# Performance work log

Hardware: AMD Instinct MI355X
Metric: run time of the kernel (lower is better)

Reference implementation:

```python
import jax, jax.numpy as jnp
import numpy as np

B, D, H = 262144, 8, 64  # batch, in_out_dim, hidden_dim


def _lin_init(k, fan_in, fan_out):
    k1, k2 = jax.random.split(k)
    s = 1.0 / np.sqrt(fan_in)
    W = jax.random.uniform(k1, (fan_in, fan_out), minval=-s, maxval=s, dtype=jnp.float32)
    b = jax.random.uniform(k2, (fan_out,), minval=-s, maxval=s, dtype=jnp.float32)
    return W, b


def setup_inputs():
    key = jax.random.key(0)
    ks = jax.random.split(key, 12)
    w1_0, b1_0 = _lin_init(ks[0], D + 1, H)
    w1_1, b1_1 = _lin_init(ks[1], H, H)
    w1_2, b1_2 = _lin_init(ks[2], H, H)
    w1_o, b1_o = _lin_init(ks[3], H, D)
    w2_0, b2_0 = _lin_init(ks[4], D + 1, H)
    w2_1, b2_1 = _lin_init(ks[5], H, H)
    w2_2, b2_2 = _lin_init(ks[6], H, H)
    w2_o, b2_o = _lin_init(ks[7], H, 1)
    t = jax.random.uniform(ks[8], (), dtype=jnp.float32)
    z = jax.random.normal(ks[9], (B, D), dtype=jnp.float32)
    logp_z = jnp.zeros((B, 1), dtype=jnp.float32)
    return dict(t=t, z=z, logp_z=logp_z,
                w1_0=w1_0, b1_0=b1_0, w1_1=w1_1, b1_1=b1_1, w1_2=w1_2, b1_2=b1_2,
                w1_o=w1_o, b1_o=b1_o,
                w2_0=w2_0, b2_0=b2_0, w2_1=w2_1, b2_1=b2_1, w2_2=w2_2, b2_2=b2_2,
                w2_o=w2_o, b2_o=b2_o)


def reference(t, z, logp_z,
              w1_0, b1_0, w1_1, b1_1, w1_2, b1_2, w1_o, b1_o,
              w2_0, b2_0, w2_1, b2_1, w2_2, b2_2, w2_o, b2_o):
    Bz, Dz = z.shape
    tcol = jnp.full((Bz, 1), t, dtype=z.dtype)  # t repeated per-sample, detached constant

    def net1(zz):  # HyperNetwork1: dz/dt field, Tanh MLP, (B,D+1)->(B,D)
        s = jnp.concatenate([tcol, zz], axis=1)
        x = jnp.tanh(s @ w1_0 + b1_0)
        x = jnp.tanh(x @ w1_1 + b1_1)
        x = jnp.tanh(x @ w1_2 + b1_2)
        return x @ w1_o + b1_o

    dz_dt = net1(z)

    # HyperNetwork2: growth term g, (B,D+1)->(B,1)
    s = jnp.concatenate([tcol, z], axis=1)
    x = jnp.tanh(s @ w2_0 + b2_0)
    x = jnp.tanh(x @ w2_1 + b2_1)
    x = jnp.tanh(x @ w2_2 + b2_2)
    g = x @ w2_o + b2_o

    # Exact trace of d(dz_dt)/dz via D forward-mode JVPs (vectorized, replaces
    # the per-dim autograd.grad loop in trace_df_dz).
    eye = jnp.eye(Dz, dtype=z.dtype)
    jv = jax.vmap(lambda e: jax.jvp(net1, (z,), (jnp.broadcast_to(e, z.shape),))[1])(eye)  # (D,B,D)
    trace = jnp.diagonal(jv, axis1=0, axis2=2).sum(-1)  # (B,)

    dlogp_z_dt = g - trace[:, None]
    return (dz_dt, dlogp_z_dt, g)
```

## Files before the change

kernel.cpp:

```cpp
#include <hip/hip_runtime.h>


#define BATCH 262144

typedef _Float16 h16;
typedef __attribute__((ext_vector_type(2))) __fp16 f16x2;
typedef __attribute__((ext_vector_type(8))) _Float16 half8;
typedef __attribute__((ext_vector_type(4))) float f32x4;

#define MFMA16(a, b, c) __builtin_amdgcn_mfma_f32_16x16x32_f16((a), (b), (c), 0, 0, 0)

#define WS_A   0
#define WS_WO  61440
#define WS_E   62464
#define WS_B   64512
#define WS_BO  66048

__device__ __forceinline__ float tanh_fast(float x) {
    float e = __builtin_amdgcn_exp2f(x * 2.8853900817779268f);
    return 1.0f - 2.0f * __builtin_amdgcn_rcpf(e + 1.0f);
}

__global__ void __launch_bounds__(256) prep(
    const float* __restrict__ w1_0, const float* __restrict__ w1_1,
    const float* __restrict__ w1_2, const float* __restrict__ w1_o,
    const float* __restrict__ w2_0, const float* __restrict__ w2_1,
    const float* __restrict__ w2_2, const float* __restrict__ w2_o,
    const float* __restrict__ b1_0, const float* __restrict__ b1_1,
    const float* __restrict__ b1_2, const float* __restrict__ b1_o,
    const float* __restrict__ b2_0, const float* __restrict__ b2_1,
    const float* __restrict__ b2_2, char* __restrict__ ws)
{
    int t = blockIdx.x * 256 + threadIdx.x;
    if (t < 3840) {
        int slot = t >> 6, lane = t & 63;
        int mrow = lane & 15, kg = lane >> 4;
        half8 v;
        #pragma unroll
        for (int kk = 0; kk < 8; ++kk) {
            int mt = 0, ks = 0;
            float val = 0.0f;
            if (slot < 4) {
                mt = slot; int k = kg * 8 + kk; int m = mt * 16 + mrow;
                val = (k < 9) ? w1_0[k * 64 + m] : 0.0f;
            } else if (slot < 12) {
                int s = slot - 4; mt = s >> 1; ks = s & 1;
                int k = ks * 32 + kg * 8 + kk; int m = mt * 16 + mrow;
                val = w1_1[k * 64 + m];
            } else if (slot < 20) {
                int s = slot - 12; mt = s >> 1; ks = s & 1;
                int k = ks * 32 + kg * 8 + kk; int m = mt * 16 + mrow;
                val = w1_2[k * 64 + m];
            } else if (slot < 22) {
                ks = slot - 20; int k = ks * 32 + kg * 8 + kk;
                val = (mrow < 8) ? w1_o[k * 8 + mrow] : 0.0f;
            } else if (slot < 26) {
                mt = slot - 22; int k = kg * 8 + kk; int m = mt * 16 + mrow;
                val = (k < 9) ? w2_0[k * 64 + m] : 0.0f;
            } else if (slot < 34) {
                int s = slot - 26; mt = s >> 1; ks = s & 1;
                int k = ks * 32 + kg * 8 + kk; int m = mt * 16 + mrow;
                val = w2_1[k * 64 + m];
            } else if (slot < 42) {
                int s = slot - 34; mt = s >> 1; ks = s & 1;
                int k = ks * 32 + kg * 8 + kk; int m = mt * 16 + mrow;
                val = w2_2[k * 64 + m];
            } else if (slot < 44) {
                ks = slot - 42; int k = ks * 32 + kg * 8 + kk;
                val = (mrow == 0) ? w2_o[k] : 0.0f;
            } else if (slot < 52) {
                int s = slot - 44; mt = s >> 1; ks = s & 1;
                int k = ks * 32 + kg * 8 + kk; int m = mt * 16 + mrow;
                val = w1_2[m * 64 + k];
            } else {
                int s = slot - 52; mt = s >> 1; ks = s & 1;
                int k = ks * 32 + kg * 8 + kk; int m = mt * 16 + mrow;
                val = w1_1[m * 64 + k];
            }
            v[kk] = (h16)val;
        }
        *(half8*)((h16*)(ws + WS_A) + (size_t)slot * 512 + (size_t)lane * 8) = v;
    } else if (t < 4352) {
        int e = t - 3840; int d = e >> 6, k = e & 63;
        ((h16*)(ws + WS_WO))[e] = (h16)w1_o[k * 8 + d];
    } else if (t < 4864) {
        int e = t - 4352; int d = e >> 6, g = (e >> 4) & 3, tr = e & 15;
        int mt = tr >> 2, r = tr & 3;
        int k = 16 * mt + 4 * g + r;
        ((float*)(ws + WS_E))[e] = w1_0[(d + 1) * 64 + k];
    } else if (t < 5248) {
        int e = t - 4864; int layer = e >> 6, i = e & 63;
        int g = i >> 4, mt = (i >> 2) & 3, r = i & 3;
        int m = 16 * mt + 4 * g + r;
        const float* bsrc = (layer == 0) ? b1_0 : (layer == 1) ? b1_1 :
                            (layer == 2) ? b1_2 : (layer == 3) ? b2_0 :
                            (layer == 4) ? b2_1 : b2_2;
        ((float*)(ws + WS_B))[e] = bsrc[m];
    } else if (t < 5264) {
        int i = t - 5248; int g = i >> 2, r = i & 3;
        int m = 4 * g + r;
        ((float*)(ws + WS_BO))[i] = (m < 8) ? b1_o[m] : 0.0f;
    }
}

__global__ void __launch_bounds__(256) cnf_mfma(
    const float* __restrict__ tp, const float* __restrict__ zp,
    const float* __restrict__ b2_o, const char* __restrict__ ws,
    float* __restrict__ out)
{
    __shared__ __align__(16) h16 xbuf[4][1024];

    const int lane = threadIdx.x & 63;
    const int wv = threadIdx.x >> 6;
    const int c = lane & 15;
    const int g = lane >> 4;
    const int sIdx = blockIdx.x * 64 + wv * 16 + c;
    const int swz = (c & 7) << 3;
    h16* xb = xbuf[wv];

    int wadr[4];
    #pragma unroll
    for (int mt = 0; mt < 4; ++mt) wadr[mt] = (c * 64 + mt * 16 + 4 * g) ^ swz;
    const int radr0 = (c * 64 + 8 * g) ^ swz;
    const int radr1 = (c * 64 + 32 + 8 * g) ^ swz;

    const h16*   wsA  = (const h16*)(ws + WS_A);
    const h16*   wsWo = (const h16*)(ws + WS_WO);
    const float* wsE  = (const float*)(ws + WS_E);
    const float* wsB  = (const float*)(ws + WS_B);
    const float* wsBo = (const float*)(ws + WS_BO);

    const float tt = tp[0];
    const f32x4 zl = *(const f32x4*)(zp + (size_t)sIdx * 8);
    const f32x4 zh = *(const f32x4*)(zp + (size_t)sIdx * 8 + 4);

    half8 b0f;
    #pragma unroll
    for (int i = 0; i < 8; ++i) b0f[i] = (h16)0.0f;
    if (g == 0) {
        b0f[0] = (h16)tt;
        b0f[1] = (h16)zl[0]; b0f[2] = (h16)zl[1]; b0f[3] = (h16)zl[2];
        b0f[4] = (h16)zl[3]; b0f[5] = (h16)zh[0]; b0f[6] = (h16)zh[1];
        b0f[7] = (h16)zh[2];
    } else if (g == 1) {
        b0f[0] = (h16)zh[3];
    }

    f32x4 d[4], t1v[4];
    f16x2 t2h[8];

    #pragma unroll
    for (int mt = 0; mt < 4; ++mt) {
        f32x4 acc = *(const f32x4*)(wsB + 0 * 64 + g * 16 + mt * 4);
        d[mt] = MFMA16(*(const half8*)(wsA + (0 + mt) * 512 + lane * 8), b0f, acc);
    }
    #pragma unroll
    for (int mt = 0; mt < 4; ++mt) {
        float x0 = tanh_fast(d[mt][0]), x1 = tanh_fast(d[mt][1]);
        float x2 = tanh_fast(d[mt][2]), x3 = tanh_fast(d[mt][3]);
        t1v[mt][0] = fmaf(-x0, x0, 1.0f); t1v[mt][1] = fmaf(-x1, x1, 1.0f);
        t1v[mt][2] = fmaf(-x2, x2, 1.0f); t1v[mt][3] = fmaf(-x3, x3, 1.0f);
        union { f16x2 h[2]; uint2 u; } pk;
        pk.h[0] = __builtin_amdgcn_cvt_pkrtz(x0, x1);
        pk.h[1] = __builtin_amdgcn_cvt_pkrtz(x2, x3);
        *(uint2*)&xb[wadr[mt]] = pk.u;
    }

    {
        half8 bf0 = *(const half8*)&xb[radr0];
        half8 bf1 = *(const half8*)&xb[radr1];
        #pragma unroll
        for (int mt = 0; mt < 4; ++mt) {
            f32x4 acc = *(const f32x4*)(wsB + 1 * 64 + g * 16 + mt * 4);
            acc = MFMA16(*(const half8*)(wsA + (4 + mt * 2) * 512 + lane * 8), bf0, acc);
            acc = MFMA16(*(const half8*)(wsA + (5 + mt * 2) * 512 + lane * 8), bf1, acc);
            d[mt] = acc;
        }
    }
    #pragma unroll
    for (int mt = 0; mt < 4; ++mt) {
        float x0 = tanh_fast(d[mt][0]), x1 = tanh_fast(d[mt][1]);
        float x2 = tanh_fast(d[mt][2]), x3 = tanh_fast(d[mt][3]);
        t2h[2 * mt]     = __builtin_amdgcn_cvt_pkrtz(fmaf(-x0, x0, 1.0f), fmaf(-x1, x1, 1.0f));
        t2h[2 * mt + 1] = __builtin_amdgcn_cvt_pkrtz(fmaf(-x2, x2, 1.0f), fmaf(-x3, x3, 1.0f));
        union { f16x2 h[2]; uint2 u; } pk;
        pk.h[0] = __builtin_amdgcn_cvt_pkrtz(x0, x1);
        pk.h[1] = __builtin_amdgcn_cvt_pkrtz(x2, x3);
        *(uint2*)&xb[wadr[mt]] = pk.u;
    }

    {
        half8 bf0 = *(const half8*)&xb[radr0];
        half8 bf1 = *(const half8*)&xb[radr1];
        #pragma unroll
        for (int mt = 0; mt < 4; ++mt) {
            f32x4 acc = *(const f32x4*)(wsB + 2 * 64 + g * 16 + mt * 4);
            acc = MFMA16(*(const half8*)(wsA + (12 + mt * 2) * 512 + lane * 8), bf0, acc);
            acc = MFMA16(*(const half8*)(wsA + (13 + mt * 2) * 512 + lane * 8), bf1, acc);
            d[mt] = acc;
        }
    }
    #pragma unroll
    for (int mt = 0; mt < 4; ++mt) {
        float x0 = tanh_fast(d[mt][0]), x1 = tanh_fast(d[mt][1]);
        float x2 = tanh_fast(d[mt][2]), x3 = tanh_fast(d[mt][3]);
        union { f16x2 h[2]; uint2 u; } pk;
        pk.h[0] = __builtin_amdgcn_cvt_pkrtz(x0, x1);
        pk.h[1] = __builtin_amdgcn_cvt_pkrtz(x2, x3);
        *(uint2*)&xb[wadr[mt]] = pk.u;
    }

    half8 gA[8];
    #pragma unroll
    for (int s = 0; s < 8; ++s)
        gA[s] = *(const half8*)(wsA + (44 + s) * 512 + lane * 8);

    half8 xf0 = *(const half8*)&xb[radr0];
    half8 xf1 = *(const half8*)&xb[radr1];

    {
        f32x4 dz = *(const f32x4*)(wsBo + g * 4);
        dz = MFMA16(*(const half8*)(wsA + 20 * 512 + lane * 8), xf0, dz);
        dz = MFMA16(*(const half8*)(wsA + 21 * 512 + lane * 8), xf1, dz);
        if (g < 2)
            *(f32x4*)(out + (size_t)sIdx * 8 + g * 4) = dz;
    }

    half8 one8;
    #pragma unroll
    for (int i = 0; i < 8; ++i) one8[i] = (h16)1.0f;
    const half8 t3f0 = one8 - xf0 * xf0;
    const half8 t3f1 = one8 - xf1 * xf1;

    f32x4 tacc[4];
    #pragma unroll
    for (int mt = 0; mt < 4; ++mt) tacc[mt] = (f32x4){0.0f, 0.0f, 0.0f, 0.0f};

    #pragma unroll 1
    for (int d0 = 0; d0 < 8; ++d0) {
        half8 w0f = *(const half8*)(wsWo + d0 * 64 + 8 * g);
        half8 w1f = *(const half8*)(wsWo + d0 * 64 + 32 + 8 * g);
        half8 sA0 = t3f0 * w0f;
        half8 sA1 = t3f1 * w1f;
        f32x4 rr[4];
        #pragma unroll
        for (int mt = 0; mt < 4; ++mt) {
            f32x4 acc = {0.0f, 0.0f, 0.0f, 0.0f};
            acc = MFMA16(gA[2 * mt], sA0, acc);
            acc = MFMA16(gA[2 * mt + 1], sA1, acc);
            rr[mt] = acc;
        }
        #pragma unroll
        for (int mt = 0; mt < 4; ++mt) {
            union { f16x2 h[2]; uint2 u; } pk;
            pk.h[0] = __builtin_amdgcn_cvt_pkrtz(rr[mt][0], rr[mt][1]) * t2h[2 * mt];
            pk.h[1] = __builtin_amdgcn_cvt_pkrtz(rr[mt][2], rr[mt][3]) * t2h[2 * mt + 1];
            *(uint2*)&xb[wadr[mt]] = pk.u;
        }
        half8 sb0 = *(const half8*)&xb[radr0];
        half8 sb1 = *(const half8*)&xb[radr1];
        #pragma unroll
        for (int mt = 0; mt < 4; ++mt) {
            f32x4 acc = {0.0f, 0.0f, 0.0f, 0.0f};
            acc = MFMA16(*(const half8*)(wsA + (52 + mt * 2) * 512 + lane * 8), sb0, acc);
            acc = MFMA16(*(const half8*)(wsA + (53 + mt * 2) * 512 + lane * 8), sb1, acc);
            f32x4 e = *(const f32x4*)(wsE + d0 * 64 + g * 16 + mt * 4);
            #pragma unroll
            for (int r = 0; r < 4; ++r) tacc[mt][r] = fmaf(acc[r], e[r], tacc[mt][r]);
        }
    }
    float tr;
    {
        f32x4 tm = tacc[0] * t1v[0];
        #pragma unroll
        for (int mt = 1; mt < 4; ++mt) {
            #pragma unroll
            for (int r = 0; r < 4; ++r) tm[r] = fmaf(tacc[mt][r], t1v[mt][r], tm[r]);
        }
        tr = tm[0] + tm[1] + tm[2] + tm[3];
    }
    tr += __shfl_xor(tr, 16);
    tr += __shfl_xor(tr, 32);

    #pragma unroll
    for (int mt = 0; mt < 4; ++mt) {
        f32x4 acc = *(const f32x4*)(wsB + 3 * 64 + g * 16 + mt * 4);
        d[mt] = MFMA16(*(const half8*)(wsA + (22 + mt) * 512 + lane * 8), b0f, acc);
    }
    #pragma unroll
    for (int mt = 0; mt < 4; ++mt) {
        union { f16x2 h[2]; uint2 u; } pk;
        pk.h[0] = __builtin_amdgcn_cvt_pkrtz(tanh_fast(d[mt][0]), tanh_fast(d[mt][1]));
        pk.h[1] = __builtin_amdgcn_cvt_pkrtz(tanh_fast(d[mt][2]), tanh_fast(d[mt][3]));
        *(uint2*)&xb[wadr[mt]] = pk.u;
    }
    #pragma unroll 1
    for (int L = 0; L < 2; ++L) {
        int sbase = (L == 0) ? 26 : 34;
        half8 bf0 = *(const half8*)&xb[radr0];
        half8 bf1 = *(const half8*)&xb[radr1];
        #pragma unroll
        for (int mt = 0; mt < 4; ++mt) {
            f32x4 acc = *(const f32x4*)(wsB + (4 + L) * 64 + g * 16 + mt * 4);
            acc = MFMA16(*(const half8*)(wsA + (sbase + mt * 2) * 512 + lane * 8), bf0, acc);
            acc = MFMA16(*(const half8*)(wsA + (sbase + mt * 2 + 1) * 512 + lane * 8), bf1, acc);
            d[mt] = acc;
        }
        #pragma unroll
        for (int mt = 0; mt < 4; ++mt) {
            union { f16x2 h[2]; uint2 u; } pk;
            pk.h[0] = __builtin_amdgcn_cvt_pkrtz(tanh_fast(d[mt][0]), tanh_fast(d[mt][1]));
            pk.h[1] = __builtin_amdgcn_cvt_pkrtz(tanh_fast(d[mt][2]), tanh_fast(d[mt][3]));
            *(uint2*)&xb[wadr[mt]] = pk.u;
        }
    }
    float gval;
    {
        half8 bf0 = *(const half8*)&xb[radr0];
        half8 bf1 = *(const half8*)&xb[radr1];
        f32x4 acc = {b2_o[0], 0.0f, 0.0f, 0.0f};
        acc = MFMA16(*(const half8*)(wsA + 42 * 512 + lane * 8), bf0, acc);
        acc = MFMA16(*(const half8*)(wsA + 43 * 512 + lane * 8), bf1, acc);
        gval = acc[0];
    }

    if (g == 0) {
        out[(size_t)BATCH * 8 + sIdx] = gval - tr;
        out[(size_t)BATCH * 9 + sIdx] = gval;
    }
}

extern "C" void kernel_launch(void* const* d_in, const int* in_sizes, int n_in,
                              void* d_out, int out_size, void* d_ws, size_t ws_size,
                              hipStream_t stream) {
    const float* tp   = (const float*)d_in[0];
    const float* zp   = (const float*)d_in[1];
    const float* w1_0 = (const float*)d_in[3];
    const float* b1_0 = (const float*)d_in[4];
    const float* w1_1 = (const float*)d_in[5];
    const float* b1_1 = (const float*)d_in[6];
    const float* w1_2 = (const float*)d_in[7];
    const float* b1_2 = (const float*)d_in[8];
    const float* w1_o = (const float*)d_in[9];
    const float* b1_o = (const float*)d_in[10];
    const float* w2_0 = (const float*)d_in[11];
    const float* b2_0 = (const float*)d_in[12];
    const float* w2_1 = (const float*)d_in[13];
    const float* b2_1 = (const float*)d_in[14];
    const float* w2_2 = (const float*)d_in[15];
    const float* b2_2 = (const float*)d_in[16];
    const float* w2_o = (const float*)d_in[17];
    const float* b2_o = (const float*)d_in[18];

    char* ws = (char*)d_ws;
    float* out = (float*)d_out;

    hipLaunchKernelGGL(prep, dim3(21), dim3(256), 0, stream,
                       w1_0, w1_1, w1_2, w1_o, w2_0, w2_1, w2_2, w2_o,
                       b1_0, b1_1, b1_2, b1_o, b2_0, b2_1, b2_2, ws);
    hipLaunchKernelGGL(cnf_mfma, dim3(BATCH / 64), dim3(256), 0, stream,
                       tp, zp, b2_o, ws, out);
}
```

Baseline: 194.8 us.

## Process two 16-sample tiles per wave to reuse weight fragments

Each wave now handles two independent 16-sample column tiles, using a doubled LDS buffer, and the grid is halved. Each weight A-fragment and bias load is shared by both tiles' MFMAs, and the two tiles give independent MFMA chains that can interleave to hide latency. The eight gA fragments that were previously held in registers across the trace loop are now reloaded from global memory inside it. Doubled accumulators and state arrays raise register pressure, which may lower occupancy.

```diff
diff --git a/kernel.cpp b/kernel.cpp
--- a/kernel.cpp
+++ b/kernel.cpp
@@ -108,15 +108,17 @@
     const float* __restrict__ b2_o, const char* __restrict__ ws,
     float* __restrict__ out)
 {
-    __shared__ __align__(16) h16 xbuf[4][1024];
+    __shared__ __align__(16) h16 xbuf[4][2][1024];
 
     const int lane = threadIdx.x & 63;
     const int wv = threadIdx.x >> 6;
     const int c = lane & 15;
     const int g = lane >> 4;
-    const int sIdx = blockIdx.x * 64 + wv * 16 + c;
     const int swz = (c & 7) << 3;
-    h16* xb = xbuf[wv];
+
+    int sIdx[2];
+    #pragma unroll
+    for (int u = 0; u < 2; ++u) sIdx[u] = blockIdx.x * 128 + wv * 32 + u * 16 + c;
 
     int wadr[4];
     #pragma unroll
@@ -131,202 +133,292 @@
     const float* wsBo = (const float*)(ws + WS_BO);
 
     const float tt = tp[0];
-    const f32x4 zl = *(const f32x4*)(zp + (size_t)sIdx * 8);
-    const f32x4 zh = *(const f32x4*)(zp + (size_t)sIdx * 8 + 4);
-
-    half8 b0f;
-    #pragma unroll
-    for (int i = 0; i < 8; ++i) b0f[i] = (h16)0.0f;
-    if (g == 0) {
-        b0f[0] = (h16)tt;
-        b0f[1] = (h16)zl[0]; b0f[2] = (h16)zl[1]; b0f[3] = (h16)zl[2];
-        b0f[4] = (h16)zl[3]; b0f[5] = (h16)zh[0]; b0f[6] = (h16)zh[1];
-        b0f[7] = (h16)zh[2];
-    } else if (g == 1) {
-        b0f[0] = (h16)zh[3];
-    }
-
-    f32x4 d[4], t1v[4];
-    f16x2 t2h[8];
+
+    half8 b0f[2];
+    #pragma unroll
+    for (int u = 0; u < 2; ++u) {
+        const f32x4 zl = *(const f32x4*)(zp + (size_t)sIdx[u] * 8);
+        const f32x4 zh = *(const f32x4*)(zp + (size_t)sIdx[u] * 8 + 4);
+        #pragma unroll
+        for (int i = 0; i < 8; ++i) b0f[u][i] = (h16)0.0f;
+        if (g == 0) {
+            b0f[u][0] = (h16)tt;
+            b0f[u][1] = (h16)zl[0]; b0f[u][2] = (h16)zl[1]; b0f[u][3] = (h16)zl[2];
+            b0f[u][4] = (h16)zl[3]; b0f[u][5] = (h16)zh[0]; b0f[u][6] = (h16)zh[1];
+            b0f[u][7] = (h16)zh[2];
+        } else if (g == 1) {
+            b0f[u][0] = (h16)zh[3];
+        }
+    }
+
+    f32x4 d[2][4], t1v[2][4];
+    f16x2 t2h[2][8];
 
     #pragma unroll
     for (int mt = 0; mt < 4; ++mt) {
-        f32x4 acc = *(const f32x4*)(wsB + 0 * 64 + g * 16 + mt * 4);
-        d[mt] = MFMA16(*(const half8*)(wsA + (0 + mt) * 512 + lane * 8), b0f, acc);
-    }
-    #pragma unroll
-    for (int mt = 0; mt < 4; ++mt) {
-        float x0 = tanh_fast(d[mt][0]), x1 = tanh_fast(d[mt][1]);
-        float x2 = tanh_fast(d[mt][2]), x3 = tanh_fast(d[mt][3]);
-        t1v[mt][0] = fmaf(-x0, x0, 1.0f); t1v[mt][1] = fmaf(-x1, x1, 1.0f);
-        t1v[mt][2] = fmaf(-x2, x2, 1.0f); t1v[mt][3] = fmaf(-x3, x3, 1.0f);
-        union { f16x2 h[2]; uint2 u; } pk;
-        pk.h[0] = __builtin_amdgcn_cvt_pkrtz(x0, x1);
-        pk.h[1] = __builtin_amdgcn_cvt_pkrtz(x2, x3);
-        *(uint2*)&xb[wadr[mt]] = pk.u;
+        half8 a = *(const half8*)(wsA + (0 + mt) * 512 + lane * 8);
+        f32x4 bias = *(const f32x4*)(wsB + 0 * 64 + g * 16 + mt * 4);
+        #pragma unroll
+        for (int u = 0; u < 2; ++u) d[u][mt] = MFMA16(a, b0f[u], bias);
+    }
+    #pragma unroll
+    for (int u = 0; u < 2; ++u) {
+        #pragma unroll
+        for (int mt = 0; mt < 4; ++mt) {
+            float x0 = tanh_fast(d[u][mt][0]), x1 = tanh_fast(d[u][mt][1]);
+            float x2 = tanh_fast(d[u][mt][2]), x3 = tanh_fast(d[u][mt][3]);
+            t1v[u][mt][0] = fmaf(-x0, x0, 1.0f); t1v[u][mt][1] = fmaf(-x1, x1, 1.0f);
+            t1v[u][mt][2] = fmaf(-x2, x2, 1.0f); t1v[u][mt][3] = fmaf(-x3, x3, 1.0f);
+            union { f16x2 h[2]; uint2 v; } pk;
+            pk.h[0] = __builtin_amdgcn_cvt_pkrtz(x0, x1);
+            pk.h[1] = __builtin_amdgcn_cvt_pkrtz(x2, x3);
+            *(uint2*)&xbuf[wv][u][wadr[mt]] = pk.v;
+        }
     }
 
     {
-        half8 bf0 = *(const half8*)&xb[radr0];
-        half8 bf1 = *(const half8*)&xb[radr1];
-        #pragma unroll
-        for (int mt = 0; mt < 4; ++mt) {
-            f32x4 acc = *(const f32x4*)(wsB + 1 * 64 + g * 16 + mt * 4);
-            acc = MFMA16(*(const half8*)(wsA + (4 + mt * 2) * 512 + lane * 8), bf0, acc);
-            acc = MFMA16(*(const half8*)(wsA + (5 + mt * 2) * 512 + lane * 8), bf1, acc);
-            d[mt] = acc;
-        }
-    }
-    #pragma unroll
-    for (int mt = 0; mt < 4; ++mt) {
-        float x0 = tanh_fast(d[mt][0]), x1 = tanh_fast(d[mt][1]);
-        float x2 = tanh_fast(d[mt][2]), x3 = tanh_fast(d[mt][3]);
-        t2h[2 * mt]     = __builtin_amdgcn_cvt_pkrtz(fmaf(-x0, x0, 1.0f), fmaf(-x1, x1, 1.0f));
-        t2h[2 * mt + 1] = __builtin_amdgcn_cvt_pkrtz(fmaf(-x2, x2, 1.0f), fmaf(-x3, x3, 1.0f));
-        union { f16x2 h[2]; uint2 u; } pk;
-        pk.h[0] = __builtin_amdgcn_cvt_pkrtz(x0, x1);
-        pk.h[1] = __builtin_amdgcn_cvt_pkrtz(x2, x3);
-        *(uint2*)&xb[wadr[mt]] = pk.u;
+        half8 bf0[2], bf1[2];
+        #pragma unroll
+        for (int u = 0; u < 2; ++u) {
+            bf0[u] = *(const half8*)&xbuf[wv][u][radr0];
+            bf1[u] = *(const half8*)&xbuf[wv][u][radr1];
+        }
+        #pragma unroll
+        for (int mt = 0; mt < 4; ++mt) {
+            half8 a0 = *(const half8*)(wsA + (4 + mt * 2) * 512 + lane * 8);
+            half8 a1 = *(const half8*)(wsA + (5 + mt * 2) * 512 + lane * 8);
+            f32x4 bias = *(const f32x4*)(wsB + 1 * 64 + g * 16 + mt * 4);
+            #pragma unroll
+            for (int u = 0; u < 2; ++u) {
+                f32x4 acc = bias;
+                acc = MFMA16(a0, bf0[u], acc);
+                acc = MFMA16(a1, bf1[u], acc);
+                d[u][mt] = acc;
+            }
+        }
+    }
+    #pragma unroll
+    for (int u = 0; u < 2; ++u) {
+        #pragma unroll
+        for (int mt = 0; mt < 4; ++mt) {
+            float x0 = tanh_fast(d[u][mt][0]), x1 = tanh_fast(d[u][mt][1]);
+            float x2 = tanh_fast(d[u][mt][2]), x3 = tanh_fast(d[u][mt][3]);
+            t2h[u][2 * mt]     = __builtin_amdgcn_cvt_pkrtz(fmaf(-x0, x0, 1.0f), fmaf(-x1, x1, 1.0f));
+            t2h[u][2 * mt + 1] = __builtin_amdgcn_cvt_pkrtz(fmaf(-x2, x2, 1.0f), fmaf(-x3, x3, 1.0f));
+            union { f16x2 h[2]; uint2 v; } pk;
+            pk.h[0] = __builtin_amdgcn_cvt_pkrtz(x0, x1);
+            pk.h[1] = __builtin_amdgcn_cvt_pkrtz(x2, x3);
+            *(uint2*)&xbuf[wv][u][wadr[mt]] = pk.v;
+        }
     }
 
     {
-        half8 bf0 = *(const half8*)&xb[radr0];
-        half8 bf1 = *(const half8*)&xb[radr1];
-        #pragma unroll
-        for (int mt = 0; mt < 4; ++mt) {
-            f32x4 acc = *(const f32x4*)(wsB + 2 * 64 + g * 16 + mt * 4);
-            acc = MFMA16(*(const half8*)(wsA + (12 + mt * 2) * 512 + lane * 8), bf0, acc);
-            acc = MFMA16(*(const half8*)(wsA + (13 + mt * 2) * 512 + lane * 8), bf1, acc);
-            d[mt] = acc;
-        }
-    }
-    #pragma unroll
-    for (int mt = 0; mt < 4; ++mt) {
-        float x0 = tanh_fast(d[mt][0]), x1 = tanh_fast(d[mt][1]);
-        float x2 = tanh_fast(d[mt][2]), x3 = tanh_fast(d[mt][3]);
-        union { f16x2 h[2]; uint2 u; } pk;
-        pk.h[0] = __builtin_amdgcn_cvt_pkrtz(x0, x1);
-        pk.h[1] = __builtin_amdgcn_cvt_pkrtz(x2, x3);
-        *(uint2*)&xb[wadr[mt]] = pk.u;
-    }
-
-    half8 gA[8];
-    #pragma unroll
-    for (int s = 0; s < 8; ++s)
-        gA[s] = *(const half8*)(wsA + (44 + s) * 512 + lane * 8);
-
-    half8 xf0 = *(const half8*)&xb[radr0];
-    half8 xf1 = *(const half8*)&xb[radr1];
+        half8 bf0[2], bf1[2];
+        #pragma unroll
+        for (int u = 0; u < 2; ++u) {
+            bf0[u] = *(const half8*)&xbuf[wv][u][radr0];
+            bf1[u] = *(const half8*)&xbuf[wv][u][radr1];
+        }
+        #pragma unroll
+        for (int mt = 0; mt < 4; ++mt) {
+            half8 a0 = *(const half8*)(wsA + (12 + mt * 2) * 512 + lane * 8);
+            half8 a1 = *(const half8*)(wsA + (13 + mt * 2) * 512 + lane * 8);
+            f32x4 bias = *(const f32x4*)(wsB + 2 * 64 + g * 16 + mt * 4);
+            #pragma unroll
+            for (int u = 0; u < 2; ++u) {
+                f32x4 acc = bias;
+                acc = MFMA16(a0, bf0[u], acc);
+                acc = MFMA16(a1, bf1[u], acc);
+                d[u][mt] = acc;
+            }
+        }
+    }
+    #pragma unroll
+    for (int u = 0; u < 2; ++u) {
+        #pragma unroll
+        for (int mt = 0; mt < 4; ++mt) {
+            float x0 = tanh_fast(d[u][mt][0]), x1 = tanh_fast(d[u][mt][1]);
+            float x2 = tanh_fast(d[u][mt][2]), x3 = tanh_fast(d[u][mt][3]);
+            union { f16x2 h[2]; uint2 v; } pk;
+            pk.h[0] = __builtin_amdgcn_cvt_pkrtz(x0, x1);
+            pk.h[1] = __builtin_amdgcn_cvt_pkrtz(x2, x3);
+            *(uint2*)&xbuf[wv][u][wadr[mt]] = pk.v;
+        }
+    }
+
+    half8 xf0[2], xf1[2];
+    #pragma unroll
+    for (int u = 0; u < 2; ++u) {
+        xf0[u] = *(const half8*)&xbuf[wv][u][radr0];
+        xf1[u] = *(const half8*)&xbuf[wv][u][radr1];
+    }
 
     {
-        f32x4 dz = *(const f32x4*)(wsBo + g * 4);
-        dz = MFMA16(*(const half8*)(wsA + 20 * 512 + lane * 8), xf0, dz);
-        dz = MFMA16(*(const half8*)(wsA + 21 * 512 + lane * 8), xf1, dz);
-        if (g < 2)
-            *(f32x4*)(out + (size_t)sIdx * 8 + g * 4) = dz;
+        half8 a0 = *(const half8*)(wsA + 20 * 512 + lane * 8);
+        half8 a1 = *(const half8*)(wsA + 21 * 512 + lane * 8);
+        f32x4 bias = *(const f32x4*)(wsBo + g * 4);
+        #pragma unroll
+        for (int u = 0; u < 2; ++u) {
+            f32x4 dz = bias;
+            dz = MFMA16(a0, xf0[u], dz);
+            dz = MFMA16(a1, xf1[u], dz);
+            if (g < 2)
+                *(f32x4*)(out + (size_t)sIdx[u] * 8 + g * 4) = dz;
+        }
     }
 
     half8 one8;
     #pragma unroll
     for (int i = 0; i < 8; ++i) one8[i] = (h16)1.0f;
-    const half8 t3f0 = one8 - xf0 * xf0;
-    const half8 t3f1 = one8 - xf1 * xf1;
-
-    f32x4 tacc[4];
-    #pragma unroll
-    for (int mt = 0; mt < 4; ++mt) tacc[mt] = (f32x4){0.0f, 0.0f, 0.0f, 0.0f};
+    half8 t3f0[2], t3f1[2];
+    #pragma unroll
+    for (int u = 0; u < 2; ++u) {
+        t3f0[u] = one8 - xf0[u] * xf0[u];
+        t3f1[u] = one8 - xf1[u] * xf1[u];
+    }
+
+    f32x4 tacc[2][4];
+    #pragma unroll
+    for (int u = 0; u < 2; ++u)
+        #pragma unroll
+        for (int mt = 0; mt < 4; ++mt) tacc[u][mt] = (f32x4){0.0f, 0.0f, 0.0f, 0.0f};
 
     #pragma unroll 1
     for (int d0 = 0; d0 < 8; ++d0) {
         half8 w0f = *(const half8*)(wsWo + d0 * 64 + 8 * g);
         half8 w1f = *(const half8*)(wsWo + d0 * 64 + 32 + 8 * g);
-        half8 sA0 = t3f0 * w0f;
-        half8 sA1 = t3f1 * w1f;
-        f32x4 rr[4];
-        #pragma unroll
-        for (int mt = 0; mt < 4; ++mt) {
-            f32x4 acc = {0.0f, 0.0f, 0.0f, 0.0f};
-            acc = MFMA16(gA[2 * mt], sA0, acc);
-            acc = MFMA16(gA[2 * mt + 1], sA1, acc);
-            rr[mt] = acc;
-        }
-        #pragma unroll
-        for (int mt = 0; mt < 4; ++mt) {
-            union { f16x2 h[2]; uint2 u; } pk;
-            pk.h[0] = __builtin_amdgcn_cvt_pkrtz(rr[mt][0], rr[mt][1]) * t2h[2 * mt];
-            pk.h[1] = __builtin_amdgcn_cvt_pkrtz(rr[mt][2], rr[mt][3]) * t2h[2 * mt + 1];
-            *(uint2*)&xb[wadr[mt]] = pk.u;
-        }
-        half8 sb0 = *(const half8*)&xb[radr0];
-        half8 sb1 = *(const half8*)&xb[radr1];
-        #pragma unroll
-        for (int mt = 0; mt < 4; ++mt) {
-            f32x4 acc = {0.0f, 0.0f, 0.0f, 0.0f};
-            acc = MFMA16(*(const half8*)(wsA + (52 + mt * 2) * 512 + lane * 8), sb0, acc);
-            acc = MFMA16(*(const half8*)(wsA + (53 + mt * 2) * 512 + lane * 8), sb1, acc);
+        half8 sA0[2], sA1[2];
+        #pragma unroll
+        for (int u = 0; u < 2; ++u) {
+            sA0[u] = t3f0[u] * w0f;
+            sA1[u] = t3f1[u] * w1f;
+        }
+        f32x4 rr[2][4];
+        #pragma unroll
+        for (int mt = 0; mt < 4; ++mt) {
+            half8 a0 = *(const half8*)(wsA + (44 + mt * 2) * 512 + lane * 8);
+            half8 a1 = *(const half8*)(wsA + (45 + mt * 2) * 512 + lane * 8);
+            #pragma unroll
+            for (int u = 0; u < 2; ++u) {
+                f32x4 acc = {0.0f, 0.0f, 0.0f, 0.0f};
+                acc = MFMA16(a0, sA0[u], acc);
+                acc = MFMA16(a1, sA1[u], acc);
+                rr[u][mt] = acc;
+            }
+        }
+        #pragma unroll
+        for (int u = 0; u < 2; ++u) {
+            #pragma unroll
+            for (int mt = 0; mt < 4; ++mt) {
+                union { f16x2 h[2]; uint2 v; } pk;
+                pk.h[0] = __builtin_amdgcn_cvt_pkrtz(rr[u][mt][0], rr[u][mt][1]) * t2h[u][2 * mt];
+                pk.h[1] = __builtin_amdgcn_cvt_pkrtz(rr[u][mt][2], rr[u][mt][3]) * t2h[u][2 * mt + 1];
+                *(uint2*)&xbuf[wv][u][wadr[mt]] = pk.v;
+            }
+        }
+        half8 sb0[2], sb1[2];
+        #pragma unroll
+        for (int u = 0; u < 2; ++u) {
+            sb0[u] = *(const half8*)&xbuf[wv][u][radr0];
+            sb1[u] = *(const half8*)&xbuf[wv][u][radr1];
+        }
+        #pragma unroll
+        for (int mt = 0; mt < 4; ++mt) {
+            half8 a0 = *(const half8*)(wsA + (52 + mt * 2) * 512 + lane * 8);
+            half8 a1 = *(const half8*)(wsA + (53 + mt * 2) * 512 + lane * 8);
             f32x4 e = *(const f32x4*)(wsE + d0 * 64 + g * 16 + mt * 4);
             #pragma unroll
-            for (int r = 0; r < 4; ++r) tacc[mt][r] = fmaf(acc[r], e[r], tacc[mt][r]);
-        }
-    }
-    float tr;
-    {
-        f32x4 tm = tacc[0] * t1v[0];
+            for (int u = 0; u < 2; ++u) {
+                f32x4 acc = {0.0f, 0.0f, 0.0f, 0.0f};
+                acc = MFMA16(a0, sb0[u], acc);
+                acc = MFMA16(a1, sb1[u], acc);
+                #pragma unroll
+                for (int r = 0; r < 4; ++r)
+                    tacc[u][mt][r] = fmaf(acc[r], e[r], tacc[u][mt][r]);
+            }
+        }
+    }
+    float tr[2];
+    #pragma unroll
+    for (int u = 0; u < 2; ++u) {
+        f32x4 tm = tacc[u][0] * t1v[u][0];
         #pragma unroll
         for (int mt = 1; mt < 4; ++mt) {
             #pragma unroll
-            for (int r = 0; r < 4; ++r) tm[r] = fmaf(tacc[mt][r], t1v[mt][r], tm[r]);
-        }
-        tr = tm[0] + tm[1] + tm[2] + tm[3];
-    }
-    tr += __shfl_xor(tr, 16);
-    tr += __shfl_xor(tr, 32);
+            for (int r = 0; r < 4; ++r) tm[r] = fmaf(tacc[u][mt][r], t1v[u][mt][r], tm[r]);
+        }
+        float t = tm[0] + tm[1] + tm[2] + tm[3];
+        t += __shfl_xor(t, 16);
+        t += __shfl_xor(t, 32);
+        tr[u] = t;
+    }
 
     #pragma unroll
     for (int mt = 0; mt < 4; ++mt) {
-        f32x4 acc = *(const f32x4*)(wsB + 3 * 64 + g * 16 + mt * 4);
-        d[mt] = MFMA16(*(const half8*)(wsA + (22 + mt) * 512 + lane * 8), b0f, acc);
-    }
-    #pragma unroll
-    for (int mt = 0; mt < 4; ++mt) {
-        union { f16x2 h[2]; uint2 u; } pk;
-        pk.h[0] = __builtin_amdgcn_cvt_pkrtz(tanh_fast(d[mt][0]), tanh_fast(d[mt][1]));
-        pk.h[1] = __builtin_amdgcn_cvt_pkrtz(tanh_fast(d[mt][2]), tanh_fast(d[mt][3]));
-        *(uint2*)&xb[wadr[mt]] = pk.u;
+        half8 a = *(const half8*)(wsA + (22 + mt) * 512 + lane * 8);
+        f32x4 bias = *(const f32x4*)(wsB + 3 * 64 + g * 16 + mt * 4);
+        #pragma unroll
+        for (int u = 0; u < 2; ++u) d[u][mt] = MFMA16(a, b0f[u], bias);
+    }
+    #pragma unroll
+    for (int u = 0; u < 2; ++u) {
+        #pragma unroll
+        for (int mt = 0; mt < 4; ++mt) {
+            union { f16x2 h[2]; uint2 v; } pk;
+            pk.h[0] = __builtin_amdgcn_cvt_pkrtz(tanh_fast(d[u][mt][0]), tanh_fast(d[u][mt][1]));
+            pk.h[1] = __builtin_amdgcn_cvt_pkrtz(tanh_fast(d[u][mt][2]), tanh_fast(d[u][mt][3]));
+            *(uint2*)&xbuf[wv][u][wadr[mt]] = pk.v;
+        }
     }
     #pragma unroll 1
     for (int L = 0; L < 2; ++L) {
         int sbase = (L == 0) ? 26 : 34;
-        half8 bf0 = *(const half8*)&xb[radr0];
-        half8 bf1 = *(const half8*)&xb[radr1];
-        #pragma unroll
-        for (int mt = 0; mt < 4; ++mt) {
-            f32x4 acc = *(const f32x4*)(wsB + (4 + L) * 64 + g * 16 + mt * 4);
-            acc = MFMA16(*(const half8*)(wsA + (sbase + mt * 2) * 512 + lane * 8), bf0, acc);
-            acc = MFMA16(*(const half8*)(wsA + (sbase + mt * 2 + 1) * 512 + lane * 8), bf1, acc);
-            d[mt] = acc;
-        }
-        #pragma unroll
-        for (int mt = 0; mt < 4; ++mt) {
-            union { f16x2 h[2]; uint2 u; } pk;
-            pk.h[0] = __builtin_amdgcn_cvt_pkrtz(tanh_fast(d[mt][0]), tanh_fast(d[mt][1]));
-            pk.h[1] = __builtin_amdgcn_cvt_pkrtz(tanh_fast(d[mt][2]), tanh_fast(d[mt][3]));
-            *(uint2*)&xb[wadr[mt]] = pk.u;
-        }
-    }
-    float gval;
+        half8 bf0[2], bf1[2];
+        #pragma unroll
+        for (int u = 0; u < 2; ++u) {
+            bf0[u] = *(const half8*)&xbuf[wv][u][radr0];
+            bf1[u] = *(const half8*)&xbuf[wv][u][radr1];
+        }
+        #pragma unroll
+        for (int mt = 0; mt < 4; ++mt) {
+            half8 a0 = *(const half8*)(wsA + (sbase + mt * 2) * 512 + lane * 8);
+            half8 a1 = *(const half8*)(wsA + (sbase + mt * 2 + 1) * 512 + lane * 8);
+            f32x4 bias = *(const f32x4*)(wsB + (4 + L) * 64 + g * 16 + mt * 4);
+            #pragma unroll
+            for (int u = 0; u < 2; ++u) {
+                f32x4 acc = bias;
+                acc = MFMA16(a0, bf0[u], acc);
+                acc = MFMA16(a1, bf1[u], acc);
+                d[u][mt] = acc;
+            }
+        }
+        #pragma unroll
+        for (int u = 0; u < 2; ++u) {
+            #pragma unroll
+            for (int mt = 0; mt < 4; ++mt) {
+                union { f16x2 h[2]; uint2 v; } pk;
+                pk.h[0] = __builtin_amdgcn_cvt_pkrtz(tanh_fast(d[u][mt][0]), tanh_fast(d[u][mt][1]));
+                pk.h[1] = __builtin_amdgcn_cvt_pkrtz(tanh_fast(d[u][mt][2]), tanh_fast(d[u][mt][3]));
+                *(uint2*)&xbuf[wv][u][wadr[mt]] = pk.v;
+            }
+        }
+    }
     {
-        half8 bf0 = *(const half8*)&xb[radr0];
-        half8 bf1 = *(const half8*)&xb[radr1];
-        f32x4 acc = {b2_o[0], 0.0f, 0.0f, 0.0f};
-        acc = MFMA16(*(const half8*)(wsA + 42 * 512 + lane * 8), bf0, acc);
-        acc = MFMA16(*(const half8*)(wsA + 43 * 512 + lane * 8), bf1, acc);
-        gval = acc[0];
-    }
-
-    if (g == 0) {
-        out[(size_t)BATCH * 8 + sIdx] = gval - tr;
-        out[(size_t)BATCH * 9 + sIdx] = gval;
+        half8 a0 = *(const half8*)(wsA + 42 * 512 + lane * 8);
+        half8 a1 = *(const half8*)(wsA + 43 * 512 + lane * 8);
+        float b2 = b2_o[0];
+        #pragma unroll
+        for (int u = 0; u < 2; ++u) {
+            half8 bf0 = *(const half8*)&xbuf[wv][u][radr0];
+            half8 bf1 = *(const half8*)&xbuf[wv][u][radr1];
+            f32x4 acc = {b2, 0.0f, 0.0f, 0.0f};
+            acc = MFMA16(a0, bf0, acc);
+            acc = MFMA16(a1, bf1, acc);
+            if (g == 0) {
+                out[(size_t)BATCH * 8 + sIdx[u]] = acc[0] - tr[u];
+                out[(size_t)BATCH * 9 + sIdx[u]] = acc[0];
+            }
+        }
     }
 }
 
@@ -358,6 +450,6 @@
     hipLaunchKernelGGL(prep, dim3(21), dim3(256), 0, stream,
                        w1_0, w1_1, w1_2, w1_o, w2_0, w2_1, w2_2, w2_o,
                        b1_0, b1_1, b1_2, b1_o, b2_0, b2_1, b2_2, ws);
-    hipLaunchKernelGGL(cnf_mfma, dim3(BATCH / 64), dim3(256), 0, stream,
+    hipLaunchKernelGGL(cnf_mfma, dim3(BATCH / 128), dim3(256), 0, stream,
                        tp, zp, b2_o, ws, out);
 }
```

Measured after the change: 208.0 us. 6.8% more time.
